# Optimization experiments

Measured on AMD Instinct MI355X. Metric: run time of the kernel, lower is better.

The kernel has to match this reference:

```python
import jax, jax.numpy as jnp
import numpy as np

N_NODES = 50000
N_EDGES = 1600000
IN_DIM = 1024
HID = 128
N_GRAPHS = 64


def setup_inputs() -> dict:
    key = jax.random.key(0)
    ks = jax.random.split(key, 8)
    x = jax.random.normal(ks[0], (N_NODES, IN_DIM), dtype=jnp.float32)
    edge_index = jax.random.randint(ks[1], (2, N_EDGES), 0, N_NODES, dtype=jnp.int32)
    batch = jnp.sort(jax.random.randint(ks[2], (N_NODES,), 0, N_GRAPHS, dtype=jnp.int32))
    # GATConv parameters (single head, concat irrelevant for 1 head)
    glorot = 1.0 / np.sqrt(IN_DIM)
    W = jax.random.uniform(ks[3], (IN_DIM, HID), minval=-glorot, maxval=glorot, dtype=jnp.float32)
    ga = 1.0 / np.sqrt(HID)
    att_src = jax.random.uniform(ks[4], (HID,), minval=-ga, maxval=ga, dtype=jnp.float32)
    att_dst = jax.random.uniform(ks[5], (HID,), minval=-ga, maxval=ga, dtype=jnp.float32)
    bias = jnp.zeros((HID,), dtype=jnp.float32)
    return {"x": x, "W": W, "att_src": att_src, "att_dst": att_dst, "bias": bias,
            "edge_index": edge_index, "batch": batch, "num_graphs": N_GRAPHS}


def reference(x, W, att_src, att_dst, bias, edge_index, batch, num_graphs):
    N = x.shape[0]
    h = x @ W                               # [N, HID]
    # add self-loops (GATConv default add_self_loops=True)
    loops = jnp.arange(N, dtype=edge_index.dtype)
    src = jnp.concatenate([edge_index[0], loops])   # [E+N]
    dst = jnp.concatenate([edge_index[1], loops])
    a_src = h @ att_src                     # [N]
    a_dst = h @ att_dst                     # [N]
    e = jax.nn.leaky_relu(a_src[src] + a_dst[dst], negative_slope=0.2)  # [E+N]
    # scatter-softmax over incoming edges of each destination node
    m = jax.ops.segment_max(e, dst, num_segments=N)
    p = jnp.exp(e - m[dst])
    denom = jax.ops.segment_sum(p, dst, num_segments=N)
    alpha = p / denom[dst]                  # [E+N]
    # attention-weighted aggregation
    out = jax.ops.segment_sum(alpha[:, None] * h[src], dst, num_segments=N)  # [N, HID]
    out = jax.nn.relu(out + bias)
    # global max pool over graphs in the batch
    return jax.ops.segment_max(out, batch, num_segments=num_graphs)          # [G, HID]
```

## Files before the change

### kernel.cpp

```cpp
#include <hip/hip_runtime.h>
#include <hip/hip_bf16.h>

#define N_NODES 50000
#define N_EDGES 1600000
#define IN_DIM 1024
#define HID 128
#define AGG_WAVES 6144

typedef __bf16 bf16x8 __attribute__((ext_vector_type(8)));
typedef float f32x4 __attribute__((ext_vector_type(4)));
typedef __bf16 bf16x4 __attribute__((ext_vector_type(4)));

__device__ __forceinline__ float2 bf2f(unsigned u) {
    return make_float2(__uint_as_float(u << 16), __uint_as_float(u & 0xffff0000u));
}
__device__ __forceinline__ float lrelu(float v) { return v > 0.f ? v : 0.2f * v; }
__device__ __forceinline__ float f16tof(unsigned bits) {
    return (float)__builtin_bit_cast(_Float16, (unsigned short)bits);
}

__global__ void prep_kernel(const float* __restrict__ W, __bf16* __restrict__ wt,
                            int* __restrict__ deg, float* __restrict__ out, int out_n) {
    int i = blockIdx.x * 256 + threadIdx.x;
    if (i < N_NODES) deg[i] = 0;
    if (i < out_n) out[i] = 0.0f;
    if (i < HID * IN_DIM) {
        int n = i >> 10, k = i & 1023;
        wt[i] = (__bf16)W[(size_t)k * HID + n];
    }
}

__global__ __launch_bounds__(256) void gemm_kernel(const float* __restrict__ x,
                                                   const __bf16* __restrict__ wt,
                                                   __bf16* __restrict__ h2,
                                                   const float* __restrict__ att_s,
                                                   const float* __restrict__ att_d,
                                                   float* __restrict__ o_as,
                                                   float* __restrict__ o_ad,
                                                   float* __restrict__ o_ps) {
    __shared__ union {
        struct { __bf16 xa[2][64][40]; __bf16 wb[2][128][40]; } s;
        __bf16 ep[64][132];
    } u;
    const int t = threadIdx.x;
    const int m0 = blockIdx.x * 64;
    const int wid = t >> 6, lane = t & 63;
    const int lm = lane & 15, q8 = (lane >> 4) * 8;
    const int rw0 = wid * 16;

    float4 xs_reg[2];
    uint2  ws_reg[4];

    auto stage_regs = [&](int k0) {
#pragma unroll
        for (int l = 0; l < 2; ++l) {
            int f = t + l * 256;
            int row = f >> 3, kq = f & 7;
            int gr = m0 + row;
            float4 v = make_float4(0.f, 0.f, 0.f, 0.f);
            if (gr < N_NODES)
                v = *(const float4*)(x + (size_t)gr * IN_DIM + k0 + kq * 4);
            xs_reg[l] = v;
        }
#pragma unroll
        for (int l = 0; l < 4; ++l) {
            int f = t + l * 256;
            int n = f >> 3, c = f & 7;
            ws_reg[l] = *(const uint2*)(wt + (size_t)n * IN_DIM + k0 + c * 4);
        }
    };
    auto regs_to_lds = [&](int b) {
#pragma unroll
        for (int l = 0; l < 2; ++l) {
            int f = t + l * 256;
            int row = f >> 3, kq = f & 7;
            bf16x4 v;
            v[0] = (__bf16)xs_reg[l].x; v[1] = (__bf16)xs_reg[l].y;
            v[2] = (__bf16)xs_reg[l].z; v[3] = (__bf16)xs_reg[l].w;
            *(bf16x4*)&u.s.xa[b][row][kq * 4] = v;
        }
#pragma unroll
        for (int l = 0; l < 4; ++l) {
            int f = t + l * 256;
            int n = f >> 3, c = f & 7;
            *(uint2*)&u.s.wb[b][n][c * 4] = ws_reg[l];
        }
    };

    f32x4 acc[8] = {};
    stage_regs(0);
    regs_to_lds(0);
    __syncthreads();
    for (int it = 0; it < 32; ++it) {
        const int cur = it & 1;
        if (it + 1 < 32) stage_regs((it + 1) * 32);
        bf16x8 af = *(const bf16x8*)&u.s.xa[cur][rw0 + lm][q8];
#pragma unroll
        for (int ct = 0; ct < 8; ++ct) {
            bf16x8 bfr = *(const bf16x8*)&u.s.wb[cur][ct * 16 + lm][q8];
            acc[ct] = __builtin_amdgcn_mfma_f32_16x16x32_bf16(af, bfr, acc[ct], 0, 0, 0);
        }
        if (it + 1 < 32) {
            regs_to_lds(cur ^ 1);
            __syncthreads();
        }
    }
    const int quad = lane >> 4;
    float attsf[8], attdf[8];
#pragma unroll
    for (int ct = 0; ct < 8; ++ct) {
        attsf[ct] = att_s[ct * 16 + lm];
        attdf[ct] = att_d[ct * 16 + lm];
    }
#pragma unroll
    for (int reg = 0; reg < 4; ++reg) {
        int row = m0 + rw0 + quad * 4 + reg;
        float ps = 0.f, pd = 0.f;
#pragma unroll
        for (int ct = 0; ct < 8; ++ct) {
            float v = acc[ct][reg];
            ps = fmaf(v, attsf[ct], ps);
            pd = fmaf(v, attdf[ct], pd);
        }
#pragma unroll
        for (int o = 8; o; o >>= 1) {
            ps += __shfl_xor(ps, o);
            pd += __shfl_xor(pd, o);
        }
        if (row < N_NODES && lm == 0) {
            o_as[row] = ps; o_ad[row] = pd;
            o_ps[row] = __expf(lrelu(ps + pd));
        }
    }
    __syncthreads();
#pragma unroll
    for (int reg = 0; reg < 4; ++reg) {
        int lrow = rw0 + quad * 4 + reg;
#pragma unroll
        for (int ct = 0; ct < 8; ++ct)
            u.ep[lrow][ct * 16 + lm] = (__bf16)acc[ct][reg];
    }
    __syncthreads();
    {
        int lr = t >> 2, qt = t & 3;
        int grow = m0 + lr;
        if (grow < N_NODES) {
            uint2* dst = (uint2*)(h2 + (size_t)grow * HID + qt * 32);
            const __bf16* srcp = &u.ep[lr][qt * 32];
#pragma unroll
            for (int j = 0; j < 8; ++j)
                dst[j] = *(const uint2*)(srcp + j * 4);
        }
    }
}

__global__ void hist_kernel(const int* __restrict__ ei, int* __restrict__ deg,
                            int* __restrict__ epos) {
    int e = blockIdx.x * 256 + threadIdx.x;
    if (e < N_EDGES) epos[e] = atomicAdd(&deg[ei[N_EDGES + e]], 1);
}

__global__ void scan1_kernel(const int* __restrict__ deg, int* __restrict__ bsum) {
    int b = blockIdx.x, t = threadIdx.x;
    int base = b * 1024 + t * 4;
    int s = 0;
#pragma unroll
    for (int j = 0; j < 4; ++j) {
        int idx = base + j;
        if (idx < N_NODES) s += deg[idx];
    }
    for (int o = 32; o; o >>= 1) s += __shfl_xor(s, o);
    __shared__ int wsum[4];
    int lane = t & 63, w = t >> 6;
    if (lane == 0) wsum[w] = s;
    __syncthreads();
    if (t == 0) bsum[b] = wsum[0] + wsum[1] + wsum[2] + wsum[3];
}

__global__ void scan2_kernel(const int* __restrict__ bsum, int* __restrict__ boff,
                             int* __restrict__ rowstart, int nb) {
    if (threadIdx.x == 0 && blockIdx.x == 0) {
        int run = 0;
        for (int i = 0; i < nb; ++i) { boff[i] = run; run += bsum[i]; }
        rowstart[N_NODES] = run;
    }
}

__global__ void scan3_kernel(const int* __restrict__ deg, const int* __restrict__ boff,
                             int* __restrict__ rowstart) {
    int b = blockIdx.x, t = threadIdx.x;
    int base = b * 1024 + t * 4;
    int v[4]; int s = 0;
#pragma unroll
    for (int j = 0; j < 4; ++j) {
        int idx = base + j;
        v[j] = (idx < N_NODES) ? deg[idx] : 0;
        s += v[j];
    }
    int lane = t & 63, w = t >> 6;
    int inc = s;
    for (int o = 1; o < 64; o <<= 1) {
        int u = __shfl_up(inc, o);
        if (lane >= o) inc += u;
    }
    __shared__ int wt[4];
    if (lane == 63) wt[w] = inc;
    __syncthreads();
    int woff = 0;
    for (int i = 0; i < w; ++i) woff += wt[i];
    int run = woff + inc - s + boff[b];
#pragma unroll
    for (int j = 0; j < 4; ++j) {
        int idx = base + j;
        if (idx < N_NODES) {
            rowstart[idx] = run;
            run += v[j];
        }
    }
}

__global__ void scatter_kernel(const int* __restrict__ ei, const int* __restrict__ rowstart,
                               const int* __restrict__ epos, unsigned* __restrict__ csrp,
                               const float* __restrict__ a_src, const float* __restrict__ a_dst) {
    int e = blockIdx.x * 256 + threadIdx.x;
    if (e >= N_EDGES) return;
    int s = ei[e], d = ei[N_EDGES + e];
    float pe = __expf(lrelu(a_src[s] + a_dst[d]));
    unsigned short hb = __builtin_bit_cast(unsigned short, (_Float16)pe);
    csrp[rowstart[d] + epos[e]] = (unsigned)s | ((unsigned)hb << 16);
}

__global__ __launch_bounds__(256, 6) void aggregate_kernel(
    const unsigned* __restrict__ h2u, const float* __restrict__ pself_a,
    const int* __restrict__ rowstart, const unsigned* __restrict__ csrp,
    const float* __restrict__ bias, const int* __restrict__ batch,
    float* __restrict__ out) {
    const int wid = threadIdx.x >> 6, lane = threadIdx.x & 63;
    const int w = blockIdx.x * 4 + wid;
    const int q = N_NODES / AGG_WAVES;
    const int r = N_NODES - q * AGG_WAVES;
    int n0 = w * q + (w < r ? w : r);
    int n1 = n0 + q + (w < r ? 1 : 0);
    const float b0 = bias[2 * lane], b1 = bias[2 * lane + 1];

    int gcur = -1;
    float m0 = 0.f, m1 = 0.f;
    for (int n = n0; n < n1; ++n) {
        int rs = rowstart[n], re = rowstart[n + 1];
        float psf = pself_a[n];
        float2 hv = bf2f(h2u[((unsigned)n << 6) | (unsigned)lane]);
        float denom = psf;
        float2 acc = make_float2(psf * hv.x, psf * hv.y);
        for (int base = rs; base < re; base += 64) {
            int cnt = re - base; if (cnt > 64) cnt = 64;
            unsigned sp = 0u;
            if (base + lane < re) sp = csrp[base + lane];
            for (int e = 0; e < cnt; e += 16) {
                unsigned bb[16], uu[16];
#pragma unroll
                for (int i = 0; i < 16; ++i) {
                    bb[i] = (unsigned)__shfl((int)sp, e + i);
                    uu[i] = h2u[((bb[i] & 0xffffu) << 6) | (unsigned)lane];
                }
#pragma unroll
                for (int i = 0; i < 16; ++i) {
                    float2 g = bf2f(uu[i]);
                    float p = f16tof(bb[i] >> 16);
                    acc.x = fmaf(p, g.x, acc.x);
                    acc.y = fmaf(p, g.y, acc.y);
                    denom += p;
                }
            }
        }
        float inv = 1.0f / denom;
        float o0 = fmaxf(fmaf(acc.x, inv, b0), 0.0f);
        float o1 = fmaxf(fmaf(acc.y, inv, b1), 0.0f);
        int g = batch[n];
        if (g != gcur) {
            if (gcur >= 0) {
                unsigned* outp = (unsigned*)(out + (size_t)gcur * HID);
                atomicMax(&outp[2 * lane], __float_as_uint(m0));
                atomicMax(&outp[2 * lane + 1], __float_as_uint(m1));
            }
            gcur = g; m0 = o0; m1 = o1;
        } else {
            m0 = fmaxf(m0, o0); m1 = fmaxf(m1, o1);
        }
    }
    if (gcur >= 0) {
        unsigned* outp = (unsigned*)(out + (size_t)gcur * HID);
        atomicMax(&outp[2 * lane], __float_as_uint(m0));
        atomicMax(&outp[2 * lane + 1], __float_as_uint(m1));
    }
}

extern "C" void kernel_launch(void* const* d_in, const int* in_sizes, int n_in,
                              void* d_out, int out_size, void* d_ws, size_t ws_size,
                              hipStream_t stream) {
    const float* x     = (const float*)d_in[0];
    const float* W     = (const float*)d_in[1];
    const float* att_s = (const float*)d_in[2];
    const float* att_d = (const float*)d_in[3];
    const float* bias  = (const float*)d_in[4];
    const int*   ei    = (const int*)d_in[5];
    const int*   batch = (const int*)d_in[6];
    float*       out   = (float*)d_out;

    char* ws = (char*)d_ws;
    size_t off = 0;
    auto alloc = [&](size_t bytes) -> void* {
        void* p = ws + off;
        off += (bytes + 255) & ~(size_t)255;
        return p;
    };
    const int NB = (N_NODES + 1023) / 1024;
    __bf16*   h2       = (__bf16*)alloc((size_t)N_NODES * HID * 2);
    __bf16*   wt       = (__bf16*)alloc((size_t)HID * IN_DIM * 2);
    float*    a_src    = (float*)alloc((size_t)N_NODES * 4);
    float*    a_dst    = (float*)alloc((size_t)N_NODES * 4);
    float*    pself    = (float*)alloc((size_t)N_NODES * 4);
    int*      deg      = (int*)alloc((size_t)N_NODES * 4);
    int*      rowstart = (int*)alloc((size_t)(N_NODES + 1) * 4);
    int*      bsum     = (int*)alloc((size_t)NB * 4);
    int*      boff     = (int*)alloc((size_t)NB * 4);
    int*      epos     = (int*)alloc((size_t)N_EDGES * 4);
    unsigned* csrp     = (unsigned*)alloc((size_t)N_EDGES * 4);
    (void)ws_size; (void)in_sizes; (void)n_in;

    hipLaunchKernelGGL(prep_kernel, dim3(512), dim3(256), 0, stream,
                       W, wt, deg, out, out_size);
    hipLaunchKernelGGL(gemm_kernel, dim3((N_NODES + 63) / 64), dim3(256), 0, stream,
                       x, wt, h2, att_s, att_d, a_src, a_dst, pself);
    hipLaunchKernelGGL(hist_kernel, dim3((N_EDGES + 255) / 256), dim3(256), 0, stream,
                       ei, deg, epos);
    hipLaunchKernelGGL(scan1_kernel, dim3(NB), dim3(256), 0, stream, deg, bsum);
    hipLaunchKernelGGL(scan2_kernel, dim3(1), dim3(64), 0, stream, bsum, boff, rowstart, NB);
    hipLaunchKernelGGL(scan3_kernel, dim3(NB), dim3(256), 0, stream, deg, boff, rowstart);
    hipLaunchKernelGGL(scatter_kernel, dim3((N_EDGES + 255) / 256), dim3(256), 0, stream,
                       ei, rowstart, epos, csrp, a_src, a_dst);
    hipLaunchKernelGGL(aggregate_kernel, dim3(AGG_WAVES / 4), dim3(256), 0, stream,
                       (const unsigned*)h2, pself, rowstart, csrp, bias, batch, out);
}
```

Before: 503.3 us.

## Enlarge GEMM row tile to 128 and merge three scan kernels into one

```diff
diff --git a/kernel.cpp b/kernel.cpp
--- a/kernel.cpp
+++ b/kernel.cpp
@@ -39,21 +39,21 @@
                                                    float* __restrict__ o_ad,
                                                    float* __restrict__ o_ps) {
     __shared__ union {
-        struct { __bf16 xa[2][64][40]; __bf16 wb[2][128][40]; } s;
-        __bf16 ep[64][132];
+        struct { __bf16 xa[2][128][40]; __bf16 wb[2][128][40]; } s;
+        __bf16 ep[128][132];
     } u;
     const int t = threadIdx.x;
-    const int m0 = blockIdx.x * 64;
+    const int m0 = blockIdx.x * 128;
     const int wid = t >> 6, lane = t & 63;
     const int lm = lane & 15, q8 = (lane >> 4) * 8;
-    const int rw0 = wid * 16;
-
-    float4 xs_reg[2];
+    const int rw0 = wid * 32;
+
+    float4 xs_reg[4];
     uint2  ws_reg[4];
 
     auto stage_regs = [&](int k0) {
 #pragma unroll
-        for (int l = 0; l < 2; ++l) {
+        for (int l = 0; l < 4; ++l) {
             int f = t + l * 256;
             int row = f >> 3, kq = f & 7;
             int gr = m0 + row;
@@ -71,7 +71,7 @@
     };
     auto regs_to_lds = [&](int b) {
 #pragma unroll
-        for (int l = 0; l < 2; ++l) {
+        for (int l = 0; l < 4; ++l) {
             int f = t + l * 256;
             int row = f >> 3, kq = f & 7;
             bf16x4 v;
@@ -87,18 +87,20 @@
         }
     };
 
-    f32x4 acc[8] = {};
+    f32x4 acc[2][8] = {};
     stage_regs(0);
     regs_to_lds(0);
     __syncthreads();
     for (int it = 0; it < 32; ++it) {
         const int cur = it & 1;
         if (it + 1 < 32) stage_regs((it + 1) * 32);
-        bf16x8 af = *(const bf16x8*)&u.s.xa[cur][rw0 + lm][q8];
+        bf16x8 af0 = *(const bf16x8*)&u.s.xa[cur][rw0 + lm][q8];
+        bf16x8 af1 = *(const bf16x8*)&u.s.xa[cur][rw0 + 16 + lm][q8];
 #pragma unroll
         for (int ct = 0; ct < 8; ++ct) {
             bf16x8 bfr = *(const bf16x8*)&u.s.wb[cur][ct * 16 + lm][q8];
-            acc[ct] = __builtin_amdgcn_mfma_f32_16x16x32_bf16(af, bfr, acc[ct], 0, 0, 0);
+            acc[0][ct] = __builtin_amdgcn_mfma_f32_16x16x32_bf16(af0, bfr, acc[0][ct], 0, 0, 0);
+            acc[1][ct] = __builtin_amdgcn_mfma_f32_16x16x32_bf16(af1, bfr, acc[1][ct], 0, 0, 0);
         }
         if (it + 1 < 32) {
             regs_to_lds(cur ^ 1);
@@ -113,42 +115,47 @@
         attdf[ct] = att_d[ct * 16 + lm];
     }
 #pragma unroll
+    for (int a = 0; a < 2; ++a) {
+#pragma unroll
+        for (int reg = 0; reg < 4; ++reg) {
+            int row = m0 + rw0 + a * 16 + quad * 4 + reg;
+            float ps = 0.f, pd = 0.f;
+#pragma unroll
+            for (int ct = 0; ct < 8; ++ct) {
+                float v = acc[a][ct][reg];
+                ps = fmaf(v, attsf[ct], ps);
+                pd = fmaf(v, attdf[ct], pd);
+            }
+#pragma unroll
+            for (int o = 8; o; o >>= 1) {
+                ps += __shfl_xor(ps, o);
+                pd += __shfl_xor(pd, o);
+            }
+            if (row < N_NODES && lm == 0) {
+                o_as[row] = ps; o_ad[row] = pd;
+                o_ps[row] = __expf(lrelu(ps + pd));
+            }
+        }
+    }
+    __syncthreads();
+#pragma unroll
+    for (int a = 0; a < 2; ++a)
+#pragma unroll
     for (int reg = 0; reg < 4; ++reg) {
-        int row = m0 + rw0 + quad * 4 + reg;
-        float ps = 0.f, pd = 0.f;
-#pragma unroll
-        for (int ct = 0; ct < 8; ++ct) {
-            float v = acc[ct][reg];
-            ps = fmaf(v, attsf[ct], ps);
-            pd = fmaf(v, attdf[ct], pd);
-        }
-#pragma unroll
-        for (int o = 8; o; o >>= 1) {
-            ps += __shfl_xor(ps, o);
-            pd += __shfl_xor(pd, o);
-        }
-        if (row < N_NODES && lm == 0) {
-            o_as[row] = ps; o_ad[row] = pd;
-            o_ps[row] = __expf(lrelu(ps + pd));
-        }
-    }
-    __syncthreads();
-#pragma unroll
-    for (int reg = 0; reg < 4; ++reg) {
-        int lrow = rw0 + quad * 4 + reg;
+        int lrow = rw0 + a * 16 + quad * 4 + reg;
 #pragma unroll
         for (int ct = 0; ct < 8; ++ct)
-            u.ep[lrow][ct * 16 + lm] = (__bf16)acc[ct][reg];
+            u.ep[lrow][ct * 16 + lm] = (__bf16)acc[a][ct][reg];
     }
     __syncthreads();
     {
-        int lr = t >> 2, qt = t & 3;
+        int lr = t >> 1, half = t & 1;
         int grow = m0 + lr;
         if (grow < N_NODES) {
-            uint2* dst = (uint2*)(h2 + (size_t)grow * HID + qt * 32);
-            const __bf16* srcp = &u.ep[lr][qt * 32];
-#pragma unroll
-            for (int j = 0; j < 8; ++j)
+            uint2* dst = (uint2*)(h2 + (size_t)grow * HID + half * 64);
+            const __bf16* srcp = &u.ep[lr][half * 64];
+#pragma unroll
+            for (int j = 0; j < 16; ++j)
                 dst[j] = *(const uint2*)(srcp + j * 4);
         }
     }
@@ -160,63 +167,34 @@
     if (e < N_EDGES) epos[e] = atomicAdd(&deg[ei[N_EDGES + e]], 1);
 }
 
-__global__ void scan1_kernel(const int* __restrict__ deg, int* __restrict__ bsum) {
-    int b = blockIdx.x, t = threadIdx.x;
-    int base = b * 1024 + t * 4;
-    int s = 0;
-#pragma unroll
-    for (int j = 0; j < 4; ++j) {
-        int idx = base + j;
-        if (idx < N_NODES) s += deg[idx];
-    }
-    for (int o = 32; o; o >>= 1) s += __shfl_xor(s, o);
-    __shared__ int wsum[4];
-    int lane = t & 63, w = t >> 6;
-    if (lane == 0) wsum[w] = s;
-    __syncthreads();
-    if (t == 0) bsum[b] = wsum[0] + wsum[1] + wsum[2] + wsum[3];
-}
-
-__global__ void scan2_kernel(const int* __restrict__ bsum, int* __restrict__ boff,
-                             int* __restrict__ rowstart, int nb) {
-    if (threadIdx.x == 0 && blockIdx.x == 0) {
-        int run = 0;
-        for (int i = 0; i < nb; ++i) { boff[i] = run; run += bsum[i]; }
-        rowstart[N_NODES] = run;
-    }
-}
-
-__global__ void scan3_kernel(const int* __restrict__ deg, const int* __restrict__ boff,
-                             int* __restrict__ rowstart) {
-    int b = blockIdx.x, t = threadIdx.x;
-    int base = b * 1024 + t * 4;
-    int v[4]; int s = 0;
-#pragma unroll
-    for (int j = 0; j < 4; ++j) {
+__global__ __launch_bounds__(1024) void scan_kernel(const int* __restrict__ deg,
+                                                    int* __restrict__ rowstart) {
+    const int t = threadIdx.x, lane = t & 63, w = t >> 6;
+    const int base = t * 49;
+    int v[49]; int s = 0;
+#pragma unroll
+    for (int j = 0; j < 49; ++j) {
         int idx = base + j;
         v[j] = (idx < N_NODES) ? deg[idx] : 0;
         s += v[j];
     }
-    int lane = t & 63, w = t >> 6;
     int inc = s;
     for (int o = 1; o < 64; o <<= 1) {
-        int u = __shfl_up(inc, o);
-        if (lane >= o) inc += u;
-    }
-    __shared__ int wt[4];
-    if (lane == 63) wt[w] = inc;
+        int u2 = __shfl_up(inc, o);
+        if (lane >= o) inc += u2;
+    }
+    __shared__ int wsum[16];
+    if (lane == 63) wsum[w] = inc;
     __syncthreads();
     int woff = 0;
-    for (int i = 0; i < w; ++i) woff += wt[i];
-    int run = woff + inc - s + boff[b];
-#pragma unroll
-    for (int j = 0; j < 4; ++j) {
+    for (int i = 0; i < w; ++i) woff += wsum[i];
+    int run = woff + inc - s;
+#pragma unroll
+    for (int j = 0; j < 49; ++j) {
         int idx = base + j;
-        if (idx < N_NODES) {
-            rowstart[idx] = run;
-            run += v[j];
-        }
-    }
+        if (idx < N_NODES) { rowstart[idx] = run; run += v[j]; }
+    }
+    if (t == 1023) rowstart[N_NODES] = run;
 }
 
 __global__ void scatter_kernel(const int* __restrict__ ei, const int* __restrict__ rowstart,
@@ -313,7 +291,6 @@
         off += (bytes + 255) & ~(size_t)255;
         return p;
     };
-    const int NB = (N_NODES + 1023) / 1024;
     __bf16*   h2       = (__bf16*)alloc((size_t)N_NODES * HID * 2);
     __bf16*   wt       = (__bf16*)alloc((size_t)HID * IN_DIM * 2);
     float*    a_src    = (float*)alloc((size_t)N_NODES * 4);
@@ -321,21 +298,17 @@
     float*    pself    = (float*)alloc((size_t)N_NODES * 4);
     int*      deg      = (int*)alloc((size_t)N_NODES * 4);
     int*      rowstart = (int*)alloc((size_t)(N_NODES + 1) * 4);
-    int*      bsum     = (int*)alloc((size_t)NB * 4);
-    int*      boff     = (int*)alloc((size_t)NB * 4);
     int*      epos     = (int*)alloc((size_t)N_EDGES * 4);
     unsigned* csrp     = (unsigned*)alloc((size_t)N_EDGES * 4);
     (void)ws_size; (void)in_sizes; (void)n_in;
 
     hipLaunchKernelGGL(prep_kernel, dim3(512), dim3(256), 0, stream,
                        W, wt, deg, out, out_size);
-    hipLaunchKernelGGL(gemm_kernel, dim3((N_NODES + 63) / 64), dim3(256), 0, stream,
+    hipLaunchKernelGGL(gemm_kernel, dim3((N_NODES + 127) / 128), dim3(256), 0, stream,
                        x, wt, h2, att_s, att_d, a_src, a_dst, pself);
     hipLaunchKernelGGL(hist_kernel, dim3((N_EDGES + 255) / 256), dim3(256), 0, stream,
                        ei, deg, epos);
-    hipLaunchKernelGGL(scan1_kernel, dim3(NB), dim3(256), 0, stream, deg, bsum);
-    hipLaunchKernelGGL(scan2_kernel, dim3(1), dim3(64), 0, stream, bsum, boff, rowstart, NB);
-    hipLaunchKernelGGL(scan3_kernel, dim3(NB), dim3(256), 0, stream, deg, boff, rowstart);
+    hipLaunchKernelGGL(scan_kernel, dim3(1), dim3(1024), 0, stream, deg, rowstart);
     hipLaunchKernelGGL(scatter_kernel, dim3((N_EDGES + 255) / 256), dim3(256), 0, stream,
                        ei, rowstart, epos, csrp, a_src, a_dst);
     hipLaunchKernelGGL(aggregate_kernel, dim3(AGG_WAVES / 4), dim3(256), 0, stream,
```

Result: slower. 571.6 us (+13.6%).
